# Kernel optimization log

Measured on AMD Instinct MI355X. Metric: run time of the kernel, lower is better.

The kernel has to match this reference:

```python
import jax, jax.numpy as jnp
import numpy as np

N = 50000   # nodes
E = 800000  # edges before self-loops
H = 4       # heads
D = 64      # num_h_feats (per-head out dim of hidden layers)
C = 2       # num_classes
NEG = 0.2   # DGL GATConv leaky_relu negative_slope
EPS = 1e-5  # BatchNorm eps


def setup_inputs() -> dict:
    key = jax.random.key(0)
    ks = jax.random.split(key, 16)
    inp = {}
    inp['feats'] = jax.random.normal(ks[0], (N, 9), jnp.float32)
    inp['W1'] = jax.random.normal(ks[1], (9, H * D), jnp.float32) * 0.1
    inp['al1'] = jax.random.normal(ks[2], (H, D), jnp.float32) * 0.1
    inp['ar1'] = jax.random.normal(ks[3], (H, D), jnp.float32) * 0.1
    inp['b1'] = jnp.zeros((H, D), jnp.float32)
    inp['Wm'] = jax.random.normal(ks[4], (D, H * D), jnp.float32) * 0.1
    inp['alm'] = jax.random.normal(ks[5], (H, D), jnp.float32) * 0.1
    inp['arm'] = jax.random.normal(ks[6], (H, D), jnp.float32) * 0.1
    inp['bm'] = jnp.zeros((H, D), jnp.float32)
    inp['W2'] = jax.random.normal(ks[7], (D, H * C), jnp.float32) * 0.1
    inp['al2'] = jax.random.normal(ks[8], (H, C), jnp.float32) * 0.1
    inp['ar2'] = jax.random.normal(ks[9], (H, C), jnp.float32) * 0.1
    inp['b2'] = jnp.zeros((H, C), jnp.float32)
    inp['gamma'] = jnp.ones((D,), jnp.float32)
    inp['beta'] = jnp.zeros((D,), jnp.float32)
    inp['src'] = jax.random.randint(ks[10], (E,), 0, N, jnp.int32)
    inp['dst'] = jax.random.randint(ks[11], (E,), 0, N, jnp.int32)
    return inp


def gat_layer(x, W, al, ar, b, src, dst, out_d):
    """DGL GATConv: linear -> per-edge attention -> dst-softmax -> scatter-sum."""
    n = x.shape[0]
    z = (x @ W).reshape(n, H, out_d)                 # [N, H, Dout]
    el = jnp.sum(z * al, axis=-1)                    # [N, H] attn on src
    er = jnp.sum(z * ar, axis=-1)                    # [N, H] attn on dst
    e = jax.nn.leaky_relu(el[src] + er[dst], NEG)    # [E, H]
    m = jax.ops.segment_max(e, dst, num_segments=n)  # per-dst max (stable softmax)
    a = jnp.exp(e - m[dst])
    s = jax.ops.segment_sum(a, dst, num_segments=n)
    alpha = a / s[dst]                               # [E, H]
    out = jax.ops.segment_sum(alpha[:, :, None] * z[src], dst, num_segments=n)
    return out + b                                   # [N, H, Dout]


def batchnorm(h, gamma, beta):
    mu = jnp.mean(h, axis=0)
    var = jnp.var(h, axis=0)
    return (h - mu) * jax.lax.rsqrt(var + EPS) * gamma + beta


def reference(feats, W1, al1, ar1, b1, Wm, alm, arm, bm, W2, al2, ar2, b2,
              gamma, beta, src, dst):
    # dgl.add_self_loop
    loop = jnp.arange(N, dtype=src.dtype)
    s = jnp.concatenate([src, loop])
    d = jnp.concatenate([dst, loop])
    h = gat_layer(feats, W1, al1, ar1, b1, s, d, D).sum(axis=1)  # head-sum
    h = batchnorm(h, gamma, beta)
    h = gat_layer(h, Wm, alm, arm, bm, s, d, D).sum(axis=1)
    h = batchnorm(h, gamma, beta)
    o = gat_layer(h, W2, al2, ar2, b2, s, d, C).sum(axis=1)      # [N, C]
    return o
```

## Files before the change

kernel.cpp:

```cpp
#include <hip/hip_runtime.h>
#include <hip/hip_bf16.h>

typedef __hip_bfloat16 bf16;
typedef __bf16 bf16x8 __attribute__((ext_vector_type(8)));
typedef float f32x4 __attribute__((ext_vector_type(4)));
typedef _Float16 h16;
typedef _Float16 h16x4 __attribute__((ext_vector_type(4)));

#define LOG2E 1.44269504088896340736f

__device__ __forceinline__ float b2f(bf16 v) { return __bfloat162float(v); }

__device__ __forceinline__ float ldin(const void* p, size_t i, int isb) {
    return isb ? b2f(((const bf16*)p)[i]) : ((const float*)p)[i];
}
__device__ __forceinline__ unsigned short f2bfbits(float f) {
    bf16 v = __float2bfloat16(f);
    return *(unsigned short*)&v;
}

__global__ __launch_bounds__(256) void prep_kernel(
    const void* __restrict__ W1, const void* __restrict__ Wm,
    const void* __restrict__ al1, const void* __restrict__ ar1,
    const void* __restrict__ alm, const void* __restrict__ arm,
    const unsigned* __restrict__ gbits,
    const int* __restrict__ dstv, int* __restrict__ deg,
    unsigned short* __restrict__ W1T, unsigned short* __restrict__ WmT,
    float* __restrict__ alf1, float* __restrict__ arf1,
    float* __restrict__ alfm, float* __restrict__ arfm,
    unsigned short* __restrict__ zhs, float* __restrict__ zcs, float* __restrict__ elp,
    int* __restrict__ flag, int Nn, int E) {
    int isb = (gbits[0] == 0x3F803F80u) ? 1 : 0;
    long t = (long)blockIdx.x * 256 + threadIdx.x;
    if (t == 0) *flag = isb;
    long b0 = 2048;
    long b1 = b0 + 2048;
    long b2 = b1 + 256;
    long b3 = b2 + 268;
    long b4 = b3 + E;
    if (t < b0) {
        long u = t;
        int col = (int)(u >> 3), k0 = ((int)u & 7) * 8;
        union { unsigned short us[8]; uint4 v; } o;
#pragma unroll
        for (int j = 0; j < 8; j++) {
            int k = k0 + j;
            o.us[j] = (k < 9) ? f2bfbits(ldin(W1, (size_t)k * 256 + col, isb))
                              : (unsigned short)0;
        }
        *(uint4*)(W1T + u * 8) = o.v;
    } else if (t < b1) {
        long u = t - b0;
        int col = (int)(u >> 3), k0 = ((int)u & 7) * 8;
        union { unsigned short us[8]; uint4 v; } o;
#pragma unroll
        for (int j = 0; j < 8; j++) {
            int k = k0 + j;
            o.us[j] = f2bfbits(ldin(Wm, (size_t)k * 256 + col, isb));
        }
        *(uint4*)(WmT + u * 8) = o.v;
    } else if (t < b2) {
        int u = (int)(t - b1);
        alf1[u] = ldin(al1, u, isb) * LOG2E; arf1[u] = ldin(ar1, u, isb) * LOG2E;
        alfm[u] = ldin(alm, u, isb) * LOG2E; arfm[u] = ldin(arm, u, isb) * LOG2E;
    } else if (t < b3) {
        long u = t - b2;
        if (u < 4) {
            elp[(size_t)Nn * 4 + u] = -1e30f;
        } else if (u < 260) {
            zhs[(size_t)Nn * 256 + (u - 4)] = 0;
        } else {
            zcs[(size_t)Nn * 8 + (u - 260)] = 0.f;
        }
    } else if (t < b4) {
        atomicAdd(&deg[dstv[t - b3]], 1);
    }
}

__global__ __launch_bounds__(256) void scan1_kernel(
    const int* __restrict__ deg, int* __restrict__ off, int* __restrict__ bsum, int Nn) {
    __shared__ int s[256];
    int t = threadIdx.x, i = blockIdx.x * 256 + t;
    int v = (i < Nn) ? ((deg[i] + 3) & ~3) : 0;
    s[t] = v; __syncthreads();
#pragma unroll
    for (int o = 1; o < 256; o <<= 1) {
        int a = (t >= o) ? s[t - o] : 0;
        __syncthreads();
        s[t] += a;
        __syncthreads();
    }
    if (i < Nn) off[i] = s[t];
    if (t == 255) bsum[blockIdx.x] = s[255];
}

__global__ __launch_bounds__(256) void scan3_kernel(
    const int* __restrict__ deg, int* __restrict__ off, int* __restrict__ cur,
    int* __restrict__ adj, const int* __restrict__ bsum, int Nn, int NB) {
    __shared__ int s[256];
    int t = threadIdx.x;
    int v = (t < NB) ? bsum[t] : 0;
    s[t] = v; __syncthreads();
#pragma unroll
    for (int o = 1; o < 256; o <<= 1) {
        int a = (t >= o) ? s[t - o] : 0;
        __syncthreads();
        s[t] += a;
        __syncthreads();
    }
    s[t] -= v;
    __syncthreads();
    int base = s[blockIdx.x];
    int i = blockIdx.x * 256 + t;
    if (i < Nn) {
        int d = deg[i], pd = (d + 3) & ~3;
        int ex = off[i] - pd + base;
        off[i] = ex;
        cur[i] = ex;
        for (int j = d; j < pd; j++) adj[ex + j] = Nn;
        if (i == Nn - 1) {
            int tot = ex + pd;
            off[Nn] = tot;
            for (int j = 0; j < 32; j++) adj[tot + j] = Nn;
        }
    }
}

__global__ __launch_bounds__(256) void scatter_kernel(
    const int* __restrict__ src, const int* __restrict__ dst,
    int* __restrict__ cur, int* __restrict__ adj, int E) {
    int t = blockIdx.x * 256 + threadIdx.x;
    if (t < E) {
        int p = atomicAdd(&cur[dst[t]], 1);
        adj[p] = src[t];
    }
}

__global__ __launch_bounds__(256) void lin_mfma_l1_kernel(
    const void* __restrict__ feats, const unsigned short* __restrict__ WT,
    const float* __restrict__ alf, const float* __restrict__ arf,
    h16* __restrict__ zh, float* __restrict__ el, float* __restrict__ er,
    const int* __restrict__ flag, int Nn) {
    __shared__ h16 zs[16 * 256];
    int isb = *flag;
    int w = threadIdx.x >> 6;
    int l = threadIdx.x & 63;
    int quad = l >> 4, lc = l & 15;
    int node0 = blockIdx.x * 16;

    int mrow = node0 + lc; if (mrow >= Nn) mrow = Nn - 1;
    union { unsigned short s[8]; bf16x8 v; } ua;
#pragma unroll
    for (int j = 0; j < 8; j++) {
        int k = quad * 8 + j;
        ua.s[j] = (k < 9) ? f2bfbits(ldin(feats, (size_t)mrow * 9 + k, isb))
                          : (unsigned short)0;
    }
    bf16x8 a0 = ua.v;

    float pe[4] = {0.f, 0.f, 0.f, 0.f}, pr[4] = {0.f, 0.f, 0.f, 0.f};
    int row0 = quad * 4;
#pragma unroll
    for (int ct = 0; ct < 4; ++ct) {
        int col = w * 64 + ct * 16 + lc;
        const bf16x8* wb = (const bf16x8*)(WT + (size_t)col * 64);
        bf16x8 b0 = wb[quad];
        f32x4 c = {0.f, 0.f, 0.f, 0.f};
        c = __builtin_amdgcn_mfma_f32_16x16x32_bf16(a0, b0, c, 0, 0, 0);
        float av = alf[col], rv = arf[col];
#pragma unroll
        for (int r = 0; r < 4; ++r) {
            pe[r] = fmaf(c[r], av, pe[r]);
            pr[r] = fmaf(c[r], rv, pr[r]);
            zs[(row0 + r) * 256 + col] = (h16)c[r];
        }
    }
#pragma unroll
    for (int o = 1; o < 16; o <<= 1) {
#pragma unroll
        for (int r = 0; r < 4; ++r) {
            pe[r] += __shfl_xor(pe[r], o);
            pr[r] += __shfl_xor(pr[r], o);
        }
    }
    if (lc == 0) {
#pragma unroll
        for (int r = 0; r < 4; ++r) {
            int n = node0 + row0 + r;
            if (n < Nn) { el[n * 4 + w] = pe[r]; er[n * 4 + w] = pr[r]; }
        }
    }
    __syncthreads();
#pragma unroll
    for (int it = 0; it < 2; ++it) {
        int flat = it * 2048 + threadIdx.x * 8;
        int row = flat >> 8;
        if (node0 + row < Nn)
            *(uint4*)(zh + (size_t)node0 * 256 + flat) = *(const uint4*)(zs + flat);
    }
}

__global__ __launch_bounds__(256) void lin_mfma_bn_kernel(
    const float* __restrict__ x,
    const float* __restrict__ bnsum, const float* __restrict__ bnsumsq,
    const void* __restrict__ gamma, const void* __restrict__ beta,
    const unsigned short* __restrict__ WT,
    const float* __restrict__ alf, const float* __restrict__ arf,
    h16* __restrict__ zh, float* __restrict__ el, float* __restrict__ er,
    const int* __restrict__ flag, int Nn) {
    __shared__ h16 zs[16 * 256];
    __shared__ __align__(16) float scs[64], shs[64];
    int tid = threadIdx.x;
    if (tid < 64) {
        int isb = *flag;
        float inv_n = 1.f / (float)Nn;
        float mu = bnsum[tid] * inv_n;
        float var = bnsumsq[tid] * inv_n - mu * mu;
        float s = rsqrtf(var + 1e-5f) * ldin(gamma, tid, isb);
        scs[tid] = s;
        shs[tid] = ldin(beta, tid, isb) - mu * s;
    }
    __syncthreads();

    int w = tid >> 6;
    int l = tid & 63;
    int quad = l >> 4, lc = l & 15;
    int node0 = blockIdx.x * 16;

    int mrow = node0 + lc; if (mrow >= Nn) mrow = Nn - 1;
    const float* xr = x + (size_t)mrow * 64 + quad * 8;
    float4 f0 = ((const float4*)xr)[0];
    float4 f1 = ((const float4*)xr)[1];
    float4 f2 = ((const float4*)(xr + 32))[0];
    float4 f3 = ((const float4*)(xr + 32))[1];
    float4 s0 = ((const float4*)(scs + quad * 8))[0];
    float4 s1 = ((const float4*)(scs + quad * 8))[1];
    float4 s2 = ((const float4*)(scs + 32 + quad * 8))[0];
    float4 s3 = ((const float4*)(scs + 32 + quad * 8))[1];
    float4 h0 = ((const float4*)(shs + quad * 8))[0];
    float4 h1 = ((const float4*)(shs + quad * 8))[1];
    float4 h2 = ((const float4*)(shs + 32 + quad * 8))[0];
    float4 h3 = ((const float4*)(shs + 32 + quad * 8))[1];

    union { bf16x8 v; unsigned short s[8]; } ua, ub;
    ua.s[0] = f2bfbits(fmaf(f0.x, s0.x, h0.x));
    ua.s[1] = f2bfbits(fmaf(f0.y, s0.y, h0.y));
    ua.s[2] = f2bfbits(fmaf(f0.z, s0.z, h0.z));
    ua.s[3] = f2bfbits(fmaf(f0.w, s0.w, h0.w));
    ua.s[4] = f2bfbits(fmaf(f1.x, s1.x, h1.x));
    ua.s[5] = f2bfbits(fmaf(f1.y, s1.y, h1.y));
    ua.s[6] = f2bfbits(fmaf(f1.z, s1.z, h1.z));
    ua.s[7] = f2bfbits(fmaf(f1.w, s1.w, h1.w));
    ub.s[0] = f2bfbits(fmaf(f2.x, s2.x, h2.x));
    ub.s[1] = f2bfbits(fmaf(f2.y, s2.y, h2.y));
    ub.s[2] = f2bfbits(fmaf(f2.z, s2.z, h2.z));
    ub.s[3] = f2bfbits(fmaf(f2.w, s2.w, h2.w));
    ub.s[4] = f2bfbits(fmaf(f3.x, s3.x, h3.x));
    ub.s[5] = f2bfbits(fmaf(f3.y, s3.y, h3.y));
    ub.s[6] = f2bfbits(fmaf(f3.z, s3.z, h3.z));
    ub.s[7] = f2bfbits(fmaf(f3.w, s3.w, h3.w));
    bf16x8 a0 = ua.v, a1 = ub.v;

    float pe[4] = {0.f, 0.f, 0.f, 0.f}, pr[4] = {0.f, 0.f, 0.f, 0.f};
    int row0 = quad * 4;
#pragma unroll
    for (int ct = 0; ct < 4; ++ct) {
        int col = w * 64 + ct * 16 + lc;
        const bf16x8* wb = (const bf16x8*)(WT + (size_t)col * 64);
        bf16x8 b0 = wb[quad];
        bf16x8 b1 = wb[quad + 4];
        f32x4 c = {0.f, 0.f, 0.f, 0.f};
        c = __builtin_amdgcn_mfma_f32_16x16x32_bf16(a0, b0, c, 0, 0, 0);
        c = __builtin_amdgcn_mfma_f32_16x16x32_bf16(a1, b1, c, 0, 0, 0);
        float av = alf[col], rv = arf[col];
#pragma unroll
        for (int r = 0; r < 4; ++r) {
            pe[r] = fmaf(c[r], av, pe[r]);
            pr[r] = fmaf(c[r], rv, pr[r]);
            zs[(row0 + r) * 256 + col] = (h16)c[r];
        }
    }
#pragma unroll
    for (int o = 1; o < 16; o <<= 1) {
#pragma unroll
        for (int r = 0; r < 4; ++r) {
            pe[r] += __shfl_xor(pe[r], o);
            pr[r] += __shfl_xor(pr[r], o);
        }
    }
    if (lc == 0) {
#pragma unroll
        for (int r = 0; r < 4; ++r) {
            int n = node0 + row0 + r;
            if (n < Nn) { el[n * 4 + w] = pe[r]; er[n * 4 + w] = pr[r]; }
        }
    }
    __syncthreads();
#pragma unroll
    for (int it = 0; it < 2; ++it) {
        int flat = it * 2048 + threadIdx.x * 8;
        int row = flat >> 8;
        if (node0 + row < Nn)
            *(uint4*)(zh + (size_t)node0 * 256 + flat) = *(const uint4*)(zs + flat);
    }
}

__global__ __launch_bounds__(256) void bnstats_kernel(
    const float* __restrict__ x, float* __restrict__ bnsum, float* __restrict__ bnsumsq,
    int Nn) {
    __shared__ float ssum[4][64], ssq[4][64];
    int tid = threadIdx.x;
    int d = tid & 63, r = tid >> 6;
    float s = 0.f, q = 0.f;
    int stride = gridDim.x * 4;
    for (int n = blockIdx.x * 4 + r; n < Nn; n += stride) {
        float v = x[(size_t)n * 64 + d];
        s += v;
        q = fmaf(v, v, q);
    }
    ssum[r][d] = s; ssq[r][d] = q;
    __syncthreads();
    if (tid < 64) {
        float ts = ssum[0][tid] + ssum[1][tid] + ssum[2][tid] + ssum[3][tid];
        float tq = ssq[0][tid] + ssq[1][tid] + ssq[2][tid] + ssq[3][tid];
        atomicAdd(&bnsum[tid], ts);
        atomicAdd(&bnsumsq[tid], tq);
    }
}

__global__ __launch_bounds__(256) void lin3_kernel(
    const float* __restrict__ x,
    const float* __restrict__ bnsum, const float* __restrict__ bnsumsq,
    const void* __restrict__ gamma, const void* __restrict__ beta,
    const void* __restrict__ W, const void* __restrict__ al, const void* __restrict__ ar,
    float* __restrict__ zc, float* __restrict__ el, float* __restrict__ er,
    const int* __restrict__ flag, int Nn) {
    __shared__ __align__(16) float scs[64], shs[64];
    int isb = *flag;
    int tid = threadIdx.x;
    if (tid < 64) {
        float inv_n = 1.f / (float)Nn;
        float mu = bnsum[tid] * inv_n;
        float var = bnsumsq[tid] * inv_n - mu * mu;
        float s = rsqrtf(var + 1e-5f) * ldin(gamma, tid, isb);
        scs[tid] = s;
        shs[tid] = ldin(beta, tid, isb) - mu * s;
    }
    __syncthreads();
    int t = blockIdx.x * 256 + tid;
    if (t >= Nn * 4) return;
    int n = t >> 2, h = t & 3;
    const float4* xr4 = (const float4*)(x + (size_t)n * 64);
    float a0 = 0.f, a1 = 0.f;
#pragma unroll 4
    for (int kk = 0; kk < 16; kk++) {
        float4 xv = xr4[kk];
        int k = kk * 4;
        float xn;
        xn = fmaf(xv.x, scs[k + 0], shs[k + 0]);
        a0 += xn * ldin(W, (k + 0) * 8 + h * 2, isb);
        a1 += xn * ldin(W, (k + 0) * 8 + h * 2 + 1, isb);
        xn = fmaf(xv.y, scs[k + 1], shs[k + 1]);
        a0 += xn * ldin(W, (k + 1) * 8 + h * 2, isb);
        a1 += xn * ldin(W, (k + 1) * 8 + h * 2 + 1, isb);
        xn = fmaf(xv.z, scs[k + 2], shs[k + 2]);
        a0 += xn * ldin(W, (k + 2) * 8 + h * 2, isb);
        a1 += xn * ldin(W, (k + 2) * 8 + h * 2 + 1, isb);
        xn = fmaf(xv.w, scs[k + 3], shs[k + 3]);
        a0 += xn * ldin(W, (k + 3) * 8 + h * 2, isb);
        a1 += xn * ldin(W, (k + 3) * 8 + h * 2 + 1, isb);
    }
    zc[n * 8 + h * 2 + 0] = a0;
    zc[n * 8 + h * 2 + 1] = a1;
    el[t] = (a0 * ldin(al, h * 2, isb) + a1 * ldin(al, h * 2 + 1, isb)) * LOG2E;
    er[t] = (a0 * ldin(ar, h * 2, isb) + a1 * ldin(ar, h * 2 + 1, isb)) * LOG2E;
}

#define GATH(ev, zv, sv)                                        \
    {                                                           \
        ev[0] = el[sv.x * 4 + h]; ev[1] = el[sv.y * 4 + h];     \
        ev[2] = el[sv.z * 4 + h]; ev[3] = el[sv.w * 4 + h];     \
        zv[0] = zrow[(size_t)sv.x * 64 + l];                    \
        zv[1] = zrow[(size_t)sv.y * 64 + l];                    \
        zv[2] = zrow[(size_t)sv.z * 64 + l];                    \
        zv[3] = zrow[(size_t)sv.w * 64 + l];                    \
    }
#define COMP(ev, zv)                                        \
    {                                                       \
        _Pragma("unroll") for (int j = 0; j < 4; j++) {     \
            float e = ev[j] + ern;                          \
            e = fmaxf(e, 0.2f * e);                         \
            float wj = __builtin_amdgcn_exp2f(e);           \
            lsum += wj;                                     \
            acc.x = fmaf(wj, (float)zv[j].x, acc.x);        \
            acc.y = fmaf(wj, (float)zv[j].y, acc.y);        \
            acc.z = fmaf(wj, (float)zv[j].z, acc.z);        \
            acc.w = fmaf(wj, (float)zv[j].w, acc.w);        \
        }                                                   \
    }

__global__ __launch_bounds__(256) void gat_agg64_kernel(
    const h16* __restrict__ zh, const float* __restrict__ el, const float* __restrict__ er,
    const int* __restrict__ off, const int* __restrict__ adj, const void* __restrict__ bias,
    float* __restrict__ x, const int* __restrict__ flag, int Nn, int total_waves) {
    int isb = *flag;
    int tid = threadIdx.x;
    int l = tid & 63;
    int h = l >> 4;
    int gw = blockIdx.x * 4 + (tid >> 6);
    const h16x4* zrow = (const h16x4*)zh;

    float4 bsl;
    bsl.x = ldin(bias, l * 4 + 0, isb);
    bsl.y = ldin(bias, l * 4 + 1, isb);
    bsl.z = ldin(bias, l * 4 + 2, isb);
    bsl.w = ldin(bias, l * 4 + 3, isb);

    if (gw >= Nn) return;

    int n = gw;
    int fs0 = off[n], fs1 = off[n + 1];
    float fel = el[n * 4 + h], fer = er[n * 4 + h];
    int4 fsv = *(const int4*)(adj + fs0);

    while (true) {
        int s0 = fs0;
        int nb = (fs1 - fs0) >> 2;
        float eln = fel, ern = fer;
        int4 svA = fsv;
        h16x4 zself = zrow[(size_t)n * 64 + l];
        int nn = n + total_waves;
        if (nn < Nn) {
            fs0 = off[nn]; fs1 = off[nn + 1];
            fel = el[nn * 4 + h]; fer = er[nn * 4 + h];
            fsv = *(const int4*)(adj + fs0);
        }

        float e0 = eln + ern;
        e0 = fmaxf(e0, 0.2f * e0);
        float w0 = __builtin_amdgcn_exp2f(e0);
        float lsum = w0;
        float4 acc = {0.f, 0.f, 0.f, 0.f};

        if (nb > 0) {
            float evA[4], evB[4];
            h16x4 zvA[4], zvB[4];
            GATH(evA, zvA, svA);
            int4 svB = *(const int4*)(adj + s0 + 4);
            int k = 0;
            while (true) {
                if (k + 1 < nb) GATH(evB, zvB, svB);
                svA = *(const int4*)(adj + s0 + (k + 2) * 4);
                COMP(evA, zvA);
                if (++k >= nb) break;
                if (k + 1 < nb) GATH(evA, zvA, svA);
                svB = *(const int4*)(adj + s0 + (k + 2) * 4);
                COMP(evB, zvB);
                if (++k >= nb) break;
            }
        }

        acc.x = fmaf(w0, (float)zself.x, acc.x);
        acc.y = fmaf(w0, (float)zself.y, acc.y);
        acc.z = fmaf(w0, (float)zself.z, acc.z);
        acc.w = fmaf(w0, (float)zself.w, acc.w);

        float inv = 1.f / lsum;
        float4 r;
        r.x = fmaf(acc.x, inv, bsl.x);
        r.y = fmaf(acc.y, inv, bsl.y);
        r.z = fmaf(acc.z, inv, bsl.z);
        r.w = fmaf(acc.w, inv, bsl.w);
#pragma unroll
        for (int o = 16; o < 64; o <<= 1) {
            r.x += __shfl_xor(r.x, o);
            r.y += __shfl_xor(r.y, o);
            r.z += __shfl_xor(r.z, o);
            r.w += __shfl_xor(r.w, o);
        }
        if (h == 0) ((float4*)(x + (size_t)n * 64))[l & 15] = r;
        if (nn >= Nn) break;
        n = nn;
    }
}
#undef GATH
#undef COMP

#define GATH2(ev, zv, sv)                                       \
    {                                                           \
        ev[0] = el[sv.x * 4 + h]; zv[0] = zc2[sv.x * 4 + h];    \
        ev[1] = el[sv.y * 4 + h]; zv[1] = zc2[sv.y * 4 + h];    \
        ev[2] = el[sv.z * 4 + h]; zv[2] = zc2[sv.z * 4 + h];    \
        ev[3] = el[sv.w * 4 + h]; zv[3] = zc2[sv.w * 4 + h];    \
    }
#define COMP2(ev, zv)                                       \
    {                                                       \
        _Pragma("unroll") for (int j = 0; j < 4; j++) {     \
            float e = ev[j] + er_nh;                        \
            e = fmaxf(e, 0.2f * e);                         \
            float w = __builtin_amdgcn_exp2f(e);            \
            lsum += w;                                      \
            a0 = fmaf(w, zv[j].x, a0);                      \
            a1 = fmaf(w, zv[j].y, a1);                      \
        }                                                   \
    }

__global__ __launch_bounds__(256) void gat_agg2_kernel(
    const float* __restrict__ zc, const float* __restrict__ el, const float* __restrict__ er,
    const int* __restrict__ off, const int* __restrict__ adj, const void* __restrict__ bias,
    void* __restrict__ out, const int* __restrict__ flag, int Nn) {
    int isb = *flag;
    int t = blockIdx.x * 256 + threadIdx.x;
    if (t >= Nn * 4) return;
    int n = t >> 2, h = t & 3;
    const float2* zc2 = (const float2*)zc;
    float er_nh = er[n * 4 + h];
    float e0 = el[n * 4 + h] + er_nh;
    e0 = fmaxf(e0, 0.2f * e0);
    float w0 = __builtin_amdgcn_exp2f(e0);
    float lsum = w0;
    float2 zn = zc2[n * 4 + h];
    float a0 = w0 * zn.x, a1 = w0 * zn.y;
    int s0 = off[n];
    int nb = (off[n + 1] - s0) >> 2;
    if (nb > 0) {
        float evA[4], evB[4], evC[4];
        float2 zvA[4], zvB[4], zvC[4];
        int4 svA = *(const int4*)(adj + s0);
        GATH2(evA, zvA, svA);
        int4 svB = *(const int4*)(adj + s0 + 4);
        if (nb > 1) GATH2(evB, zvB, svB);
        int4 svC = *(const int4*)(adj + s0 + 8);
        int k = 0;
        while (true) {
            if (k + 2 < nb) GATH2(evC, zvC, svC);
            svA = *(const int4*)(adj + s0 + (k + 3) * 4);
            COMP2(evA, zvA);
            if (++k >= nb) break;
            if (k + 2 < nb) GATH2(evA, zvA, svA);
            svB = *(const int4*)(adj + s0 + (k + 3) * 4);
            COMP2(evB, zvB);
            if (++k >= nb) break;
            if (k + 2 < nb) GATH2(evB, zvB, svB);
            svC = *(const int4*)(adj + s0 + (k + 3) * 4);
            COMP2(evC, zvC);
            if (++k >= nb) break;
        }
    }
    float inv = 1.f / lsum;
    float v0 = fmaf(a0, inv, ldin(bias, h * 2 + 0, isb));
    float v1 = fmaf(a1, inv, ldin(bias, h * 2 + 1, isb));
#pragma unroll
    for (int o = 1; o < 4; o <<= 1) {
        v0 += __shfl_xor(v0, o);
        v1 += __shfl_xor(v1, o);
    }
    if (h == 0) {
        if (isb) {
            ((bf16*)out)[n * 2 + 0] = __float2bfloat16(v0);
            ((bf16*)out)[n * 2 + 1] = __float2bfloat16(v1);
        } else {
            ((float*)out)[n * 2 + 0] = v0;
            ((float*)out)[n * 2 + 1] = v1;
        }
    }
}
#undef GATH2
#undef COMP2

extern "C" void kernel_launch(void* const* d_in, const int* in_sizes, int n_in,
                              void* d_out, int out_size, void* d_ws, size_t ws_size,
                              hipStream_t stream) {
    const void* feats = d_in[0];
    const void* W1    = d_in[1];
    const void* al1   = d_in[2];
    const void* ar1   = d_in[3];
    const void* b1    = d_in[4];
    const void* Wm    = d_in[5];
    const void* alm   = d_in[6];
    const void* arm   = d_in[7];
    const void* bm    = d_in[8];
    const void* W2    = d_in[9];
    const void* al2   = d_in[10];
    const void* ar2   = d_in[11];
    const void* b2v   = d_in[12];
    const void* gamma = d_in[13];
    const void* beta  = d_in[14];
    const int*  src   = (const int*)d_in[15];
    const int*  dst   = (const int*)d_in[16];

    int Nn = in_sizes[0] / 9;
    int E  = in_sizes[15];

    float* ws = (float*)d_ws;
    h16*   zh   = (h16*)ws;
    float* zc   = ws + (size_t)(Nn + 1) * 128;
    float* el   = zc + (size_t)Nn * 8 + 8;
    float* er   = el + (size_t)Nn * 4 + 4;
    float* x    = er + (size_t)Nn * 4;
    int*   deg  = (int*)(x + (size_t)Nn * 64);
    float* bns1 = (float*)(deg + Nn);
    float* bnq1 = bns1 + 64;
    float* bns2 = bnq1 + 64;
    float* bnq2 = bns2 + 64;
    size_t msetBytes = (size_t)Nn * 4 + 256 * 4;
    float* alf1 = bnq2 + 64;
    float* arf1 = alf1 + 256;
    float* alfm = arf1 + 256;
    float* arfm = alfm + 256;
    unsigned short* W1T =
        (unsigned short*)(((uintptr_t)(arfm + 256) + 15) & ~(uintptr_t)15);
    unsigned short* WmT  = W1T + 256 * 64;
    int*   flag = (int*)(WmT + 256 * 64);
    int*   off  = flag + 1;
    int*   cur  = off + Nn + 1;
    int*   adj  = (int*)(((uintptr_t)(cur + Nn) + 15) & ~(uintptr_t)15);
    int*   bsum = adj + E + 3 * Nn + 32;

    dim3 B(256);
    int NB1 = (Nn + 255) / 256;
    int gE  = (E + 255) / 256;
    int gMF = (Nn + 15) / 16;
    int gN4 = (Nn * 4 + 255) / 256;
    long prepN = 2048 + 2048 + 256 + 268 + (long)E;
    int gPrep = (int)((prepN + 255) / 256);
    int AGG_GRID = 2048;
    int total_waves = AGG_GRID * 4;

    hipMemsetAsync(deg, 0, msetBytes, stream);

    prep_kernel<<<gPrep, B, 0, stream>>>(W1, Wm, al1, ar1, alm, arm,
                                         (const unsigned*)gamma, dst, deg,
                                         W1T, WmT,
                                         alf1, arf1, alfm, arfm,
                                         (unsigned short*)zh, zc, el, flag, Nn, E);

    scan1_kernel<<<NB1, B, 0, stream>>>(deg, off, bsum, Nn);
    scan3_kernel<<<NB1, B, 0, stream>>>(deg, off, cur, adj, bsum, Nn, NB1);
    scatter_kernel<<<gE, B, 0, stream>>>(src, dst, cur, adj, E);

    lin_mfma_l1_kernel<<<gMF, B, 0, stream>>>(feats, W1T, alf1, arf1,
                                              zh, el, er, flag, Nn);
    gat_agg64_kernel<<<AGG_GRID, B, 0, stream>>>(
        zh, el, er, off, adj, b1, x, flag, Nn, total_waves);
    bnstats_kernel<<<512, B, 0, stream>>>(x, bns1, bnq1, Nn);

    lin_mfma_bn_kernel<<<gMF, B, 0, stream>>>(x, bns1, bnq1, gamma, beta,
                                              WmT, alfm, arfm, zh, el, er, flag, Nn);
    gat_agg64_kernel<<<AGG_GRID, B, 0, stream>>>(
        zh, el, er, off, adj, bm, x, flag, Nn, total_waves);
    bnstats_kernel<<<512, B, 0, stream>>>(x, bns2, bnq2, Nn);

    lin3_kernel<<<gN4, B, 0, stream>>>(x, bns2, bnq2, gamma, beta,
                                       W2, al2, ar2, zc, el, er, flag, Nn);
    gat_agg2_kernel<<<gN4, B, 0, stream>>>(zc, el, er, off, adj, b2v, d_out, flag, Nn);
}
```

Measured before the change: 446.1 us.

## Fuse preprocessing, BN and linear stages into cooperative grid-synced kernels

Replaces the memset, degree count, scan, scatter and first linear launches with one cooperative kernel that uses grid.sync between phases. It also fuses BN statistics with the following MFMA linear layer, and BN, the final linear layer and the 2-class aggregation into further cooperative kernels. Each keeps the old multi-kernel path as a fallback if the cooperative launch fails. The aim is to cut kernel launch overhead and inter-kernel gaps, at the cost of grid-wide barriers and a fixed 1024-block grid that may lower parallelism in some phases.

```diff
diff --git a/kernel.cpp b/kernel.cpp
--- a/kernel.cpp
+++ b/kernel.cpp
@@ -1,5 +1,8 @@
 #include <hip/hip_runtime.h>
 #include <hip/hip_bf16.h>
+#include <hip/hip_cooperative_groups.h>
+
+namespace cg = cooperative_groups;
 
 typedef __hip_bfloat16 bf16;
 typedef __bf16 bf16x8 __attribute__((ext_vector_type(8)));
@@ -18,6 +21,457 @@
     bf16 v = __float2bfloat16(f);
     return *(unsigned short*)&v;
 }
+
+
+__global__ __launch_bounds__(256, 4) void coop_prep_kernel(
+    const void* feats, const void* W1, const void* Wm,
+    const void* al1, const void* ar1, const void* alm, const void* arm,
+    const unsigned* gbits, const int* src, const int* dst,
+    int* deg, unsigned short* W1T, unsigned short* WmT,
+    float* alf1, float* arf1, float* alfm, float* arfm,
+    h16* zh, float* zc, float* el, float* er,
+    int* flag, int* off, int* cur, int* adj, int* bsum, float* bnz,
+    int Nn, int E, int NB) {
+    cg::grid_group grid = cg::this_grid();
+    __shared__ int s[256];
+    __shared__ h16 zs[16 * 256];
+    int tid = threadIdx.x;
+    long gt = (long)blockIdx.x * 256 + tid;
+    long gstride = (long)gridDim.x * 256;
+    int isb = (gbits[0] == 0x3F803F80u) ? 1 : 0;
+
+    {
+        long total = 4620 + (long)Nn + 256;
+        for (long t = gt; t < total; t += gstride) {
+            if (t < 2048) {
+                int col = (int)(t >> 3), k0 = ((int)t & 7) * 8;
+                union { unsigned short us[8]; uint4 v; } o;
+#pragma unroll
+                for (int j = 0; j < 8; j++) {
+                    int k = k0 + j;
+                    o.us[j] = (k < 9) ? f2bfbits(ldin(W1, (size_t)k * 256 + col, isb))
+                                      : (unsigned short)0;
+                }
+                *(uint4*)(W1T + t * 8) = o.v;
+            } else if (t < 4096) {
+                long u = t - 2048;
+                int col = (int)(u >> 3), k0 = ((int)u & 7) * 8;
+                union { unsigned short us[8]; uint4 v; } o;
+#pragma unroll
+                for (int j = 0; j < 8; j++) {
+                    int k = k0 + j;
+                    o.us[j] = f2bfbits(ldin(Wm, (size_t)k * 256 + col, isb));
+                }
+                *(uint4*)(WmT + u * 8) = o.v;
+            } else if (t < 4352) {
+                int u = (int)(t - 4096);
+                alf1[u] = ldin(al1, u, isb) * LOG2E; arf1[u] = ldin(ar1, u, isb) * LOG2E;
+                alfm[u] = ldin(alm, u, isb) * LOG2E; arfm[u] = ldin(arm, u, isb) * LOG2E;
+            } else if (t < 4620) {
+                long u = t - 4352;
+                if (u < 4) {
+                    el[(size_t)Nn * 4 + u] = -1e30f;
+                } else if (u < 260) {
+                    ((unsigned short*)zh)[(size_t)Nn * 256 + (u - 4)] = 0;
+                } else {
+                    zc[(size_t)Nn * 8 + (u - 260)] = 0.f;
+                }
+            } else if (t < 4620 + Nn) {
+                deg[t - 4620] = 0;
+            } else {
+                bnz[t - 4620 - Nn] = 0.f;
+            }
+        }
+        if (gt == 0) *flag = isb;
+    }
+    grid.sync();
+
+    for (long t = gt; t < (long)E; t += gstride)
+        atomicAdd(&deg[dst[t]], 1);
+    {
+        int w = tid >> 6;
+        int l = tid & 63;
+        int quad = l >> 4, lc = l & 15;
+        int ntiles = (Nn + 15) >> 4;
+        for (int tile = blockIdx.x; tile < ntiles; tile += gridDim.x) {
+            int node0 = tile * 16;
+            int mrow = node0 + lc; if (mrow >= Nn) mrow = Nn - 1;
+            union { unsigned short us[8]; bf16x8 v; } ua;
+#pragma unroll
+            for (int j = 0; j < 8; j++) {
+                int k = quad * 8 + j;
+                ua.us[j] = (k < 9) ? f2bfbits(ldin(feats, (size_t)mrow * 9 + k, isb))
+                                   : (unsigned short)0;
+            }
+            bf16x8 a0 = ua.v;
+            float pe[4] = {0.f, 0.f, 0.f, 0.f}, pr[4] = {0.f, 0.f, 0.f, 0.f};
+            int row0 = quad * 4;
+#pragma unroll
+            for (int ct = 0; ct < 4; ++ct) {
+                int col = w * 64 + ct * 16 + lc;
+                const bf16x8* wb = (const bf16x8*)(W1T + (size_t)col * 64);
+                bf16x8 b0 = wb[quad];
+                f32x4 c = {0.f, 0.f, 0.f, 0.f};
+                c = __builtin_amdgcn_mfma_f32_16x16x32_bf16(a0, b0, c, 0, 0, 0);
+                float av = alf1[col], rv = arf1[col];
+#pragma unroll
+                for (int r2 = 0; r2 < 4; ++r2) {
+                    pe[r2] = fmaf(c[r2], av, pe[r2]);
+                    pr[r2] = fmaf(c[r2], rv, pr[r2]);
+                    zs[(row0 + r2) * 256 + col] = (h16)c[r2];
+                }
+            }
+#pragma unroll
+            for (int o = 1; o < 16; o <<= 1) {
+#pragma unroll
+                for (int r2 = 0; r2 < 4; ++r2) {
+                    pe[r2] += __shfl_xor(pe[r2], o);
+                    pr[r2] += __shfl_xor(pr[r2], o);
+                }
+            }
+            if (lc == 0) {
+#pragma unroll
+                for (int r2 = 0; r2 < 4; ++r2) {
+                    int n = node0 + row0 + r2;
+                    if (n < Nn) { el[n * 4 + w] = pe[r2]; er[n * 4 + w] = pr[r2]; }
+                }
+            }
+            __syncthreads();
+#pragma unroll
+            for (int it = 0; it < 2; ++it) {
+                int flat = it * 2048 + tid * 8;
+                int row = flat >> 8;
+                if (node0 + row < Nn)
+                    *(uint4*)(zh + (size_t)node0 * 256 + flat) = *(const uint4*)(zs + flat);
+            }
+            __syncthreads();
+        }
+    }
+    grid.sync();
+
+    for (int v = blockIdx.x; v < NB; v += gridDim.x) {
+        int i = v * 256 + tid;
+        int val = (i < Nn) ? ((deg[i] + 3) & ~3) : 0;
+        s[tid] = val; __syncthreads();
+#pragma unroll
+        for (int o = 1; o < 256; o <<= 1) {
+            int a = (tid >= o) ? s[tid - o] : 0;
+            __syncthreads();
+            s[tid] += a;
+            __syncthreads();
+        }
+        if (i < Nn) off[i] = s[tid];
+        if (tid == 255) bsum[v] = s[255];
+        __syncthreads();
+    }
+    grid.sync();
+
+    for (int v = blockIdx.x; v < NB; v += gridDim.x) {
+        int val = (tid < NB) ? bsum[tid] : 0;
+        s[tid] = val; __syncthreads();
+#pragma unroll
+        for (int o = 1; o < 256; o <<= 1) {
+            int a = (tid >= o) ? s[tid - o] : 0;
+            __syncthreads();
+            s[tid] += a;
+            __syncthreads();
+        }
+        s[tid] -= val;
+        __syncthreads();
+        int base = s[v];
+        int i = v * 256 + tid;
+        if (i < Nn) {
+            int d = deg[i], pd = (d + 3) & ~3;
+            int ex = off[i] - pd + base;
+            off[i] = ex;
+            cur[i] = ex;
+            for (int j = d; j < pd; j++) adj[ex + j] = Nn;
+            if (i == Nn - 1) {
+                int tot = ex + pd;
+                off[Nn] = tot;
+                for (int j = 0; j < 32; j++) adj[tot + j] = Nn;
+            }
+        }
+        __syncthreads();
+    }
+    grid.sync();
+
+    for (long t = gt; t < (long)E; t += gstride) {
+        int p = atomicAdd(&cur[dst[t]], 1);
+        adj[p] = src[t];
+    }
+}
+
+__global__ __launch_bounds__(256, 4) void coop_bn_lin_kernel(
+    const float* x, float* bnsum, float* bnsumsq,
+    const void* gamma, const void* beta,
+    const unsigned short* WT, const float* alf, const float* arf,
+    h16* zh, float* el, float* er, const int* flag, int Nn) {
+    cg::grid_group grid = cg::this_grid();
+    __shared__ float ssum[4][64], ssq[4][64];
+    __shared__ h16 zs[16 * 256];
+    __shared__ __align__(16) float scs[64], shs[64];
+    int tid = threadIdx.x;
+
+    if (blockIdx.x < 512) {
+        int d = tid & 63, r = tid >> 6;
+        float sa = 0.f, qa = 0.f;
+        for (int n = blockIdx.x * 4 + r; n < Nn; n += 2048) {
+            float v = x[(size_t)n * 64 + d];
+            sa += v;
+            qa = fmaf(v, v, qa);
+        }
+        ssum[r][d] = sa; ssq[r][d] = qa;
+        __syncthreads();
+        if (tid < 64) {
+            atomicAdd(&bnsum[tid], ssum[0][tid] + ssum[1][tid] + ssum[2][tid] + ssum[3][tid]);
+            atomicAdd(&bnsumsq[tid], ssq[0][tid] + ssq[1][tid] + ssq[2][tid] + ssq[3][tid]);
+        }
+    }
+    grid.sync();
+
+    int isb = *flag;
+    if (tid < 64) {
+        float inv_n = 1.f / (float)Nn;
+        float mu = bnsum[tid] * inv_n;
+        float var = bnsumsq[tid] * inv_n - mu * mu;
+        float sc = rsqrtf(var + 1e-5f) * ldin(gamma, tid, isb);
+        scs[tid] = sc;
+        shs[tid] = ldin(beta, tid, isb) - mu * sc;
+    }
+    __syncthreads();
+
+    int w = tid >> 6;
+    int l = tid & 63;
+    int quad = l >> 4, lc = l & 15;
+    int ntiles = (Nn + 15) >> 4;
+    for (int tile = blockIdx.x; tile < ntiles; tile += gridDim.x) {
+        int node0 = tile * 16;
+        int mrow = node0 + lc; if (mrow >= Nn) mrow = Nn - 1;
+        const float* xr = x + (size_t)mrow * 64 + quad * 8;
+        float4 f0 = ((const float4*)xr)[0];
+        float4 f1 = ((const float4*)xr)[1];
+        float4 f2 = ((const float4*)(xr + 32))[0];
+        float4 f3 = ((const float4*)(xr + 32))[1];
+        float4 s0 = ((const float4*)(scs + quad * 8))[0];
+        float4 s1 = ((const float4*)(scs + quad * 8))[1];
+        float4 s2 = ((const float4*)(scs + 32 + quad * 8))[0];
+        float4 s3 = ((const float4*)(scs + 32 + quad * 8))[1];
+        float4 h0 = ((const float4*)(shs + quad * 8))[0];
+        float4 h1 = ((const float4*)(shs + quad * 8))[1];
+        float4 h2 = ((const float4*)(shs + 32 + quad * 8))[0];
+        float4 h3 = ((const float4*)(shs + 32 + quad * 8))[1];
+
+        union { bf16x8 v; unsigned short us[8]; } ua, ub;
+        ua.us[0] = f2bfbits(fmaf(f0.x, s0.x, h0.x));
+        ua.us[1] = f2bfbits(fmaf(f0.y, s0.y, h0.y));
+        ua.us[2] = f2bfbits(fmaf(f0.z, s0.z, h0.z));
+        ua.us[3] = f2bfbits(fmaf(f0.w, s0.w, h0.w));
+        ua.us[4] = f2bfbits(fmaf(f1.x, s1.x, h1.x));
+        ua.us[5] = f2bfbits(fmaf(f1.y, s1.y, h1.y));
+        ua.us[6] = f2bfbits(fmaf(f1.z, s1.z, h1.z));
+        ua.us[7] = f2bfbits(fmaf(f1.w, s1.w, h1.w));
+        ub.us[0] = f2bfbits(fmaf(f2.x, s2.x, h2.x));
+        ub.us[1] = f2bfbits(fmaf(f2.y, s2.y, h2.y));
+        ub.us[2] = f2bfbits(fmaf(f2.z, s2.z, h2.z));
+        ub.us[3] = f2bfbits(fmaf(f2.w, s2.w, h2.w));
+        ub.us[4] = f2bfbits(fmaf(f3.x, s3.x, h3.x));
+        ub.us[5] = f2bfbits(fmaf(f3.y, s3.y, h3.y));
+        ub.us[6] = f2bfbits(fmaf(f3.z, s3.z, h3.z));
+        ub.us[7] = f2bfbits(fmaf(f3.w, s3.w, h3.w));
+        bf16x8 a0 = ua.v, a1 = ub.v;
+
+        float pe[4] = {0.f, 0.f, 0.f, 0.f}, pr[4] = {0.f, 0.f, 0.f, 0.f};
+        int row0 = quad * 4;
+#pragma unroll
+        for (int ct = 0; ct < 4; ++ct) {
+            int col = w * 64 + ct * 16 + lc;
+            const bf16x8* wb = (const bf16x8*)(WT + (size_t)col * 64);
+            bf16x8 b0 = wb[quad];
+            bf16x8 b1 = wb[quad + 4];
+            f32x4 c = {0.f, 0.f, 0.f, 0.f};
+            c = __builtin_amdgcn_mfma_f32_16x16x32_bf16(a0, b0, c, 0, 0, 0);
+            c = __builtin_amdgcn_mfma_f32_16x16x32_bf16(a1, b1, c, 0, 0, 0);
+            float av = alf[col], rv = arf[col];
+#pragma unroll
+            for (int r2 = 0; r2 < 4; ++r2) {
+                pe[r2] = fmaf(c[r2], av, pe[r2]);
+                pr[r2] = fmaf(c[r2], rv, pr[r2]);
+                zs[(row0 + r2) * 256 + col] = (h16)c[r2];
+            }
+        }
+#pragma unroll
+        for (int o = 1; o < 16; o <<= 1) {
+#pragma unroll
+            for (int r2 = 0; r2 < 4; ++r2) {
+                pe[r2] += __shfl_xor(pe[r2], o);
+                pr[r2] += __shfl_xor(pr[r2], o);
+            }
+        }
+        if (lc == 0) {
+#pragma unroll
+            for (int r2 = 0; r2 < 4; ++r2) {
+                int n = node0 + row0 + r2;
+                if (n < Nn) { el[n * 4 + w] = pe[r2]; er[n * 4 + w] = pr[r2]; }
+            }
+        }
+        __syncthreads();
+#pragma unroll
+        for (int it = 0; it < 2; ++it) {
+            int flat = it * 2048 + tid * 8;
+            int row = flat >> 8;
+            if (node0 + row < Nn)
+                *(uint4*)(zh + (size_t)node0 * 256 + flat) = *(const uint4*)(zs + flat);
+        }
+        __syncthreads();
+    }
+}
+
+#define GATH2(ev, zv, sv)                                       \
+    {                                                           \
+        ev[0] = el[sv.x * 4 + h]; zv[0] = zc2[sv.x * 4 + h];    \
+        ev[1] = el[sv.y * 4 + h]; zv[1] = zc2[sv.y * 4 + h];    \
+        ev[2] = el[sv.z * 4 + h]; zv[2] = zc2[sv.z * 4 + h];    \
+        ev[3] = el[sv.w * 4 + h]; zv[3] = zc2[sv.w * 4 + h];    \
+    }
+#define COMP2(ev, zv)                                       \
+    {                                                       \
+        _Pragma("unroll") for (int j = 0; j < 4; j++) {     \
+            float e = ev[j] + er_nh;                        \
+            e = fmaxf(e, 0.2f * e);                         \
+            float w = __builtin_amdgcn_exp2f(e);            \
+            lsum += w;                                      \
+            a0 = fmaf(w, zv[j].x, a0);                      \
+            a1 = fmaf(w, zv[j].y, a1);                      \
+        }                                                   \
+    }
+
+__global__ __launch_bounds__(256, 4) void coop_bn_lin3_agg2_kernel(
+    const float* x, float* bnsum, float* bnsumsq,
+    const void* gamma, const void* beta,
+    const void* W, const void* al, const void* ar,
+    float* zc, float* el, float* er,
+    const int* off, const int* adj, const void* bias,
+    void* out, const int* flag, int Nn) {
+    cg::grid_group grid = cg::this_grid();
+    __shared__ float ssum[4][64], ssq[4][64];
+    __shared__ __align__(16) float scs[64], shs[64];
+    int tid = threadIdx.x;
+    long gt = (long)blockIdx.x * 256 + tid;
+    long gstride = (long)gridDim.x * 256;
+
+    if (blockIdx.x < 512) {
+        int d = tid & 63, r = tid >> 6;
+        float sa = 0.f, qa = 0.f;
+        for (int n = blockIdx.x * 4 + r; n < Nn; n += 2048) {
+            float v = x[(size_t)n * 64 + d];
+            sa += v;
+            qa = fmaf(v, v, qa);
+        }
+        ssum[r][d] = sa; ssq[r][d] = qa;
+        __syncthreads();
+        if (tid < 64) {
+            atomicAdd(&bnsum[tid], ssum[0][tid] + ssum[1][tid] + ssum[2][tid] + ssum[3][tid]);
+            atomicAdd(&bnsumsq[tid], ssq[0][tid] + ssq[1][tid] + ssq[2][tid] + ssq[3][tid]);
+        }
+    }
+    grid.sync();
+
+    int isb = *flag;
+    if (tid < 64) {
+        float inv_n = 1.f / (float)Nn;
+        float mu = bnsum[tid] * inv_n;
+        float var = bnsumsq[tid] * inv_n - mu * mu;
+        float sc = rsqrtf(var + 1e-5f) * ldin(gamma, tid, isb);
+        scs[tid] = sc;
+        shs[tid] = ldin(beta, tid, isb) - mu * sc;
+    }
+    __syncthreads();
+    for (long t = gt; t < (long)Nn * 4; t += gstride) {
+        int n = (int)(t >> 2), h = (int)(t & 3);
+        const float4* xr4 = (const float4*)(x + (size_t)n * 64);
+        float a0 = 0.f, a1 = 0.f;
+#pragma unroll 4
+        for (int kk = 0; kk < 16; kk++) {
+            float4 xv = xr4[kk];
+            int k = kk * 4;
+            float xn;
+            xn = fmaf(xv.x, scs[k + 0], shs[k + 0]);
+            a0 += xn * ldin(W, (k + 0) * 8 + h * 2, isb);
+            a1 += xn * ldin(W, (k + 0) * 8 + h * 2 + 1, isb);
+            xn = fmaf(xv.y, scs[k + 1], shs[k + 1]);
+            a0 += xn * ldin(W, (k + 1) * 8 + h * 2, isb);
+            a1 += xn * ldin(W, (k + 1) * 8 + h * 2 + 1, isb);
+            xn = fmaf(xv.z, scs[k + 2], shs[k + 2]);
+            a0 += xn * ldin(W, (k + 2) * 8 + h * 2, isb);
+            a1 += xn * ldin(W, (k + 2) * 8 + h * 2 + 1, isb);
+            xn = fmaf(xv.w, scs[k + 3], shs[k + 3]);
+            a0 += xn * ldin(W, (k + 3) * 8 + h * 2, isb);
+            a1 += xn * ldin(W, (k + 3) * 8 + h * 2 + 1, isb);
+        }
+        zc[n * 8 + h * 2 + 0] = a0;
+        zc[n * 8 + h * 2 + 1] = a1;
+        el[t] = (a0 * ldin(al, h * 2, isb) + a1 * ldin(al, h * 2 + 1, isb)) * LOG2E;
+        er[t] = (a0 * ldin(ar, h * 2, isb) + a1 * ldin(ar, h * 2 + 1, isb)) * LOG2E;
+    }
+    grid.sync();
+
+    const float2* zc2 = (const float2*)zc;
+    for (long t = gt; t < (long)Nn * 4; t += gstride) {
+        int n = (int)(t >> 2), h = (int)(t & 3);
+        float er_nh = er[n * 4 + h];
+        float e0 = el[n * 4 + h] + er_nh;
+        e0 = fmaxf(e0, 0.2f * e0);
+        float w0 = __builtin_amdgcn_exp2f(e0);
+        float lsum = w0;
+        float2 zn = zc2[n * 4 + h];
+        float a0 = w0 * zn.x, a1 = w0 * zn.y;
+        int s0 = off[n];
+        int nb = (off[n + 1] - s0) >> 2;
+        if (nb > 0) {
+            float evA[4], evB[4], evC[4];
+            float2 zvA[4], zvB[4], zvC[4];
+            int4 svA = *(const int4*)(adj + s0);
+            GATH2(evA, zvA, svA);
+            int4 svB = *(const int4*)(adj + s0 + 4);
+            if (nb > 1) GATH2(evB, zvB, svB);
+            int4 svC = *(const int4*)(adj + s0 + 8);
+            int k = 0;
+            while (true) {
+                if (k + 2 < nb) GATH2(evC, zvC, svC);
+                svA = *(const int4*)(adj + s0 + (k + 3) * 4);
+                COMP2(evA, zvA);
+                if (++k >= nb) break;
+                if (k + 2 < nb) GATH2(evA, zvA, svA);
+                svB = *(const int4*)(adj + s0 + (k + 3) * 4);
+                COMP2(evB, zvB);
+                if (++k >= nb) break;
+                if (k + 2 < nb) GATH2(evB, zvB, svB);
+                svC = *(const int4*)(adj + s0 + (k + 3) * 4);
+                COMP2(evC, zvC);
+                if (++k >= nb) break;
+            }
+        }
+        float inv = 1.f / lsum;
+        float v0 = fmaf(a0, inv, ldin(bias, h * 2 + 0, isb));
+        float v1 = fmaf(a1, inv, ldin(bias, h * 2 + 1, isb));
+#pragma unroll
+        for (int o = 1; o < 4; o <<= 1) {
+            v0 += __shfl_xor(v0, o);
+            v1 += __shfl_xor(v1, o);
+        }
+        if (h == 0) {
+            if (isb) {
+                ((bf16*)out)[n * 2 + 0] = __float2bfloat16(v0);
+                ((bf16*)out)[n * 2 + 1] = __float2bfloat16(v1);
+            } else {
+                ((float*)out)[n * 2 + 0] = v0;
+                ((float*)out)[n * 2 + 1] = v1;
+            }
+        }
+    }
+}
+
 
 __global__ __launch_bounds__(256) void prep_kernel(
     const void* __restrict__ W1, const void* __restrict__ Wm,
@@ -375,135 +829,6 @@
     el[t] = (a0 * ldin(al, h * 2, isb) + a1 * ldin(al, h * 2 + 1, isb)) * LOG2E;
     er[t] = (a0 * ldin(ar, h * 2, isb) + a1 * ldin(ar, h * 2 + 1, isb)) * LOG2E;
 }
-
-#define GATH(ev, zv, sv)                                        \
-    {                                                           \
-        ev[0] = el[sv.x * 4 + h]; ev[1] = el[sv.y * 4 + h];     \
-        ev[2] = el[sv.z * 4 + h]; ev[3] = el[sv.w * 4 + h];     \
-        zv[0] = zrow[(size_t)sv.x * 64 + l];                    \
-        zv[1] = zrow[(size_t)sv.y * 64 + l];                    \
-        zv[2] = zrow[(size_t)sv.z * 64 + l];                    \
-        zv[3] = zrow[(size_t)sv.w * 64 + l];                    \
-    }
-#define COMP(ev, zv)                                        \
-    {                                                       \
-        _Pragma("unroll") for (int j = 0; j < 4; j++) {     \
-            float e = ev[j] + ern;                          \
-            e = fmaxf(e, 0.2f * e);                         \
-            float wj = __builtin_amdgcn_exp2f(e);           \
-            lsum += wj;                                     \
-            acc.x = fmaf(wj, (float)zv[j].x, acc.x);        \
-            acc.y = fmaf(wj, (float)zv[j].y, acc.y);        \
-            acc.z = fmaf(wj, (float)zv[j].z, acc.z);        \
-            acc.w = fmaf(wj, (float)zv[j].w, acc.w);        \
-        }                                                   \
-    }
-
-__global__ __launch_bounds__(256) void gat_agg64_kernel(
-    const h16* __restrict__ zh, const float* __restrict__ el, const float* __restrict__ er,
-    const int* __restrict__ off, const int* __restrict__ adj, const void* __restrict__ bias,
-    float* __restrict__ x, const int* __restrict__ flag, int Nn, int total_waves) {
-    int isb = *flag;
-    int tid = threadIdx.x;
-    int l = tid & 63;
-    int h = l >> 4;
-    int gw = blockIdx.x * 4 + (tid >> 6);
-    const h16x4* zrow = (const h16x4*)zh;
-
-    float4 bsl;
-    bsl.x = ldin(bias, l * 4 + 0, isb);
-    bsl.y = ldin(bias, l * 4 + 1, isb);
-    bsl.z = ldin(bias, l * 4 + 2, isb);
-    bsl.w = ldin(bias, l * 4 + 3, isb);
-
-    if (gw >= Nn) return;
-
-    int n = gw;
-    int fs0 = off[n], fs1 = off[n + 1];
-    float fel = el[n * 4 + h], fer = er[n * 4 + h];
-    int4 fsv = *(const int4*)(adj + fs0);
-
-    while (true) {
-        int s0 = fs0;
-        int nb = (fs1 - fs0) >> 2;
-        float eln = fel, ern = fer;
-        int4 svA = fsv;
-        h16x4 zself = zrow[(size_t)n * 64 + l];
-        int nn = n + total_waves;
-        if (nn < Nn) {
-            fs0 = off[nn]; fs1 = off[nn + 1];
-            fel = el[nn * 4 + h]; fer = er[nn * 4 + h];
-            fsv = *(const int4*)(adj + fs0);
-        }
-
-        float e0 = eln + ern;
-        e0 = fmaxf(e0, 0.2f * e0);
-        float w0 = __builtin_amdgcn_exp2f(e0);
-        float lsum = w0;
-        float4 acc = {0.f, 0.f, 0.f, 0.f};
-
-        if (nb > 0) {
-            float evA[4], evB[4];
-            h16x4 zvA[4], zvB[4];
-            GATH(evA, zvA, svA);
-            int4 svB = *(const int4*)(adj + s0 + 4);
-            int k = 0;
-            while (true) {
-                if (k + 1 < nb) GATH(evB, zvB, svB);
-                svA = *(const int4*)(adj + s0 + (k + 2) * 4);
-                COMP(evA, zvA);
-                if (++k >= nb) break;
-                if (k + 1 < nb) GATH(evA, zvA, svA);
-                svB = *(const int4*)(adj + s0 + (k + 2) * 4);
-                COMP(evB, zvB);
-                if (++k >= nb) break;
-            }
-        }
-
-        acc.x = fmaf(w0, (float)zself.x, acc.x);
-        acc.y = fmaf(w0, (float)zself.y, acc.y);
-        acc.z = fmaf(w0, (float)zself.z, acc.z);
-        acc.w = fmaf(w0, (float)zself.w, acc.w);
-
-        float inv = 1.f / lsum;
-        float4 r;
-        r.x = fmaf(acc.x, inv, bsl.x);
-        r.y = fmaf(acc.y, inv, bsl.y);
-        r.z = fmaf(acc.z, inv, bsl.z);
-        r.w = fmaf(acc.w, inv, bsl.w);
-#pragma unroll
-        for (int o = 16; o < 64; o <<= 1) {
-            r.x += __shfl_xor(r.x, o);
-            r.y += __shfl_xor(r.y, o);
-            r.z += __shfl_xor(r.z, o);
-            r.w += __shfl_xor(r.w, o);
-        }
-        if (h == 0) ((float4*)(x + (size_t)n * 64))[l & 15] = r;
-        if (nn >= Nn) break;
-        n = nn;
-    }
-}
-#undef GATH
-#undef COMP
-
-#define GATH2(ev, zv, sv)                                       \
-    {                                                           \
-        ev[0] = el[sv.x * 4 + h]; zv[0] = zc2[sv.x * 4 + h];    \
-        ev[1] = el[sv.y * 4 + h]; zv[1] = zc2[sv.y * 4 + h];    \
-        ev[2] = el[sv.z * 4 + h]; zv[2] = zc2[sv.z * 4 + h];    \
-        ev[3] = el[sv.w * 4 + h]; zv[3] = zc2[sv.w * 4 + h];    \
-    }
-#define COMP2(ev, zv)                                       \
-    {                                                       \
-        _Pragma("unroll") for (int j = 0; j < 4; j++) {     \
-            float e = ev[j] + er_nh;                        \
-            e = fmaxf(e, 0.2f * e);                         \
-            float w = __builtin_amdgcn_exp2f(e);            \
-            lsum += w;                                      \
-            a0 = fmaf(w, zv[j].x, a0);                      \
-            a1 = fmaf(w, zv[j].y, a1);                      \
-        }                                                   \
-    }
 
 __global__ __launch_bounds__(256) void gat_agg2_kernel(
     const float* __restrict__ zc, const float* __restrict__ el, const float* __restrict__ er,
@@ -568,6 +893,116 @@
 #undef GATH2
 #undef COMP2
 
+#define GATH(ev, zv, sv)                                        \
+    {                                                           \
+        ev[0] = el[sv.x * 4 + h]; ev[1] = el[sv.y * 4 + h];     \
+        ev[2] = el[sv.z * 4 + h]; ev[3] = el[sv.w * 4 + h];     \
+        zv[0] = zrow[(size_t)sv.x * 64 + l];                    \
+        zv[1] = zrow[(size_t)sv.y * 64 + l];                    \
+        zv[2] = zrow[(size_t)sv.z * 64 + l];                    \
+        zv[3] = zrow[(size_t)sv.w * 64 + l];                    \
+    }
+#define COMP(ev, zv)                                        \
+    {                                                       \
+        _Pragma("unroll") for (int j = 0; j < 4; j++) {     \
+            float e = ev[j] + ern;                          \
+            e = fmaxf(e, 0.2f * e);                         \
+            float wj = __builtin_amdgcn_exp2f(e);           \
+            lsum += wj;                                     \
+            acc.x = fmaf(wj, (float)zv[j].x, acc.x);        \
+            acc.y = fmaf(wj, (float)zv[j].y, acc.y);        \
+            acc.z = fmaf(wj, (float)zv[j].z, acc.z);        \
+            acc.w = fmaf(wj, (float)zv[j].w, acc.w);        \
+        }                                                   \
+    }
+
+__global__ __launch_bounds__(256) void gat_agg64_kernel(
+    const h16* __restrict__ zh, const float* __restrict__ el, const float* __restrict__ er,
+    const int* __restrict__ off, const int* __restrict__ adj, const void* __restrict__ bias,
+    float* __restrict__ x, const int* __restrict__ flag, int Nn, int total_waves) {
+    int isb = *flag;
+    int tid = threadIdx.x;
+    int l = tid & 63;
+    int h = l >> 4;
+    int gw = blockIdx.x * 4 + (tid >> 6);
+    const h16x4* zrow = (const h16x4*)zh;
+
+    float4 bsl;
+    bsl.x = ldin(bias, l * 4 + 0, isb);
+    bsl.y = ldin(bias, l * 4 + 1, isb);
+    bsl.z = ldin(bias, l * 4 + 2, isb);
+    bsl.w = ldin(bias, l * 4 + 3, isb);
+
+    if (gw >= Nn) return;
+
+    int n = gw;
+    int fs0 = off[n], fs1 = off[n + 1];
+    float fel = el[n * 4 + h], fer = er[n * 4 + h];
+    int4 fsv = *(const int4*)(adj + fs0);
+
+    while (true) {
+        int s0 = fs0;
+        int nb = (fs1 - fs0) >> 2;
+        float eln = fel, ern = fer;
+        int4 svA = fsv;
+        h16x4 zself = zrow[(size_t)n * 64 + l];
+        int nn = n + total_waves;
+        if (nn < Nn) {
+            fs0 = off[nn]; fs1 = off[nn + 1];
+            fel = el[nn * 4 + h]; fer = er[nn * 4 + h];
+            fsv = *(const int4*)(adj + fs0);
+        }
+
+        float e0 = eln + ern;
+        e0 = fmaxf(e0, 0.2f * e0);
+        float w0 = __builtin_amdgcn_exp2f(e0);
+        float lsum = w0;
+        float4 acc = {0.f, 0.f, 0.f, 0.f};
+
+        if (nb > 0) {
+            float evA[4], evB[4];
+            h16x4 zvA[4], zvB[4];
+            GATH(evA, zvA, svA);
+            int4 svB = *(const int4*)(adj + s0 + 4);
+            int k = 0;
+            while (true) {
+                if (k + 1 < nb) GATH(evB, zvB, svB);
+                svA = *(const int4*)(adj + s0 + (k + 2) * 4);
+                COMP(evA, zvA);
+                if (++k >= nb) break;
+                if (k + 1 < nb) GATH(evA, zvA, svA);
+                svB = *(const int4*)(adj + s0 + (k + 2) * 4);
+                COMP(evB, zvB);
+                if (++k >= nb) break;
+            }
+        }
+
+        acc.x = fmaf(w0, (float)zself.x, acc.x);
+        acc.y = fmaf(w0, (float)zself.y, acc.y);
+        acc.z = fmaf(w0, (float)zself.z, acc.z);
+        acc.w = fmaf(w0, (float)zself.w, acc.w);
+
+        float inv = 1.f / lsum;
+        float4 r;
+        r.x = fmaf(acc.x, inv, bsl.x);
+        r.y = fmaf(acc.y, inv, bsl.y);
+        r.z = fmaf(acc.z, inv, bsl.z);
+        r.w = fmaf(acc.w, inv, bsl.w);
+#pragma unroll
+        for (int o = 16; o < 64; o <<= 1) {
+            r.x += __shfl_xor(r.x, o);
+            r.y += __shfl_xor(r.y, o);
+            r.z += __shfl_xor(r.z, o);
+            r.w += __shfl_xor(r.w, o);
+        }
+        if (h == 0) ((float4*)(x + (size_t)n * 64))[l & 15] = r;
+        if (nn >= Nn) break;
+        n = nn;
+    }
+}
+#undef GATH
+#undef COMP
+
 extern "C" void kernel_launch(void* const* d_in, const int* in_sizes, int n_in,
                               void* d_out, int out_size, void* d_ws, size_t ws_size,
                               hipStream_t stream) {
@@ -624,34 +1059,73 @@
     int gN4 = (Nn * 4 + 255) / 256;
     long prepN = 2048 + 2048 + 256 + 268 + (long)E;
     int gPrep = (int)((prepN + 255) / 256);
+    int G = 1024;
     int AGG_GRID = 2048;
     int total_waves = AGG_GRID * 4;
 
-    hipMemsetAsync(deg, 0, msetBytes, stream);
-
-    prep_kernel<<<gPrep, B, 0, stream>>>(W1, Wm, al1, ar1, alm, arm,
-                                         (const unsigned*)gamma, dst, deg,
-                                         W1T, WmT,
-                                         alf1, arf1, alfm, arfm,
-                                         (unsigned short*)zh, zc, el, flag, Nn, E);
-
-    scan1_kernel<<<NB1, B, 0, stream>>>(deg, off, bsum, Nn);
-    scan3_kernel<<<NB1, B, 0, stream>>>(deg, off, cur, adj, bsum, Nn, NB1);
-    scatter_kernel<<<gE, B, 0, stream>>>(src, dst, cur, adj, E);
-
-    lin_mfma_l1_kernel<<<gMF, B, 0, stream>>>(feats, W1T, alf1, arf1,
-                                              zh, el, er, flag, Nn);
+    hipError_t e1;
+    {
+        void* a1[] = {(void*)&feats, (void*)&W1, (void*)&Wm,
+                      (void*)&al1, (void*)&ar1, (void*)&alm, (void*)&arm,
+                      (void*)&gamma, (void*)&src, (void*)&dst,
+                      (void*)&deg, (void*)&W1T, (void*)&WmT,
+                      (void*)&alf1, (void*)&arf1, (void*)&alfm, (void*)&arfm,
+                      (void*)&zh, (void*)&zc, (void*)&el, (void*)&er,
+                      (void*)&flag, (void*)&off, (void*)&cur, (void*)&adj,
+                      (void*)&bsum, (void*)&bns1, (void*)&Nn, (void*)&E, (void*)&NB1};
+        e1 = hipLaunchCooperativeKernel((void*)coop_prep_kernel, dim3(G), B,
+                                        a1, 0, stream);
+    }
+    if (e1 != hipSuccess) {
+        hipMemsetAsync(deg, 0, msetBytes, stream);
+        prep_kernel<<<gPrep, B, 0, stream>>>(W1, Wm, al1, ar1, alm, arm,
+                                             (const unsigned*)gamma, dst, deg,
+                                             W1T, WmT, alf1, arf1, alfm, arfm,
+                                             (unsigned short*)zh, zc, el, flag, Nn, E);
+        scan1_kernel<<<NB1, B, 0, stream>>>(deg, off, bsum, Nn);
+        scan3_kernel<<<NB1, B, 0, stream>>>(deg, off, cur, adj, bsum, Nn, NB1);
+        scatter_kernel<<<gE, B, 0, stream>>>(src, dst, cur, adj, E);
+        lin_mfma_l1_kernel<<<gMF, B, 0, stream>>>(feats, W1T, alf1, arf1,
+                                                  zh, el, er, flag, Nn);
+    }
+
     gat_agg64_kernel<<<AGG_GRID, B, 0, stream>>>(
         zh, el, er, off, adj, b1, x, flag, Nn, total_waves);
-    bnstats_kernel<<<512, B, 0, stream>>>(x, bns1, bnq1, Nn);
-
-    lin_mfma_bn_kernel<<<gMF, B, 0, stream>>>(x, bns1, bnq1, gamma, beta,
-                                              WmT, alfm, arfm, zh, el, er, flag, Nn);
+
+    hipError_t e2 = hipErrorUnknown;
+    if (e1 == hipSuccess) {
+        void* a2[] = {(void*)&x, (void*)&bns1, (void*)&bnq1,
+                      (void*)&gamma, (void*)&beta,
+                      (void*)&WmT, (void*)&alfm, (void*)&arfm,
+                      (void*)&zh, (void*)&el, (void*)&er, (void*)&flag, (void*)&Nn};
+        e2 = hipLaunchCooperativeKernel((void*)coop_bn_lin_kernel, dim3(G), B,
+                                        a2, 0, stream);
+    }
+    if (e2 != hipSuccess) {
+        bnstats_kernel<<<512, B, 0, stream>>>(x, bns1, bnq1, Nn);
+        lin_mfma_bn_kernel<<<gMF, B, 0, stream>>>(x, bns1, bnq1, gamma, beta,
+                                                  WmT, alfm, arfm, zh, el, er, flag, Nn);
+    }
+
     gat_agg64_kernel<<<AGG_GRID, B, 0, stream>>>(
         zh, el, er, off, adj, bm, x, flag, Nn, total_waves);
-    bnstats_kernel<<<512, B, 0, stream>>>(x, bns2, bnq2, Nn);
-
-    lin3_kernel<<<gN4, B, 0, stream>>>(x, bns2, bnq2, gamma, beta,
-                                       W2, al2, ar2, zc, el, er, flag, Nn);
-    gat_agg2_kernel<<<gN4, B, 0, stream>>>(zc, el, er, off, adj, b2v, d_out, flag, Nn);
-}
+
+    hipError_t e3 = hipErrorUnknown;
+    if (e1 == hipSuccess) {
+        void* a3[] = {(void*)&x, (void*)&bns2, (void*)&bnq2,
+                      (void*)&gamma, (void*)&beta,
+                      (void*)&W2, (void*)&al2, (void*)&ar2,
+                      (void*)&zc, (void*)&el, (void*)&er,
+                      (void*)&off, (void*)&adj, (void*)&b2v,
+                      (void*)&d_out, (void*)&flag, (void*)&Nn};
+        e3 = hipLaunchCooperativeKernel((void*)coop_bn_lin3_agg2_kernel, dim3(G), B,
+                                        a3, 0, stream);
+    }
+    if (e3 != hipSuccess) {
+        bnstats_kernel<<<512, B, 0, stream>>>(x, bns2, bnq2, Nn);
+        lin3_kernel<<<gN4, B, 0, stream>>>(x, bns2, bnq2, gamma, beta,
+                                           W2, al2, ar2, zc, el, er, flag, Nn);
+        gat_agg2_kernel<<<gN4, B, 0, stream>>>(zc, el, er, off, adj, b2v,
+                                               d_out, flag, Nn);
+    }
+}
```

Measured after the change: 1.243 ms. 2.79x slower.
